# Performance work log

Measured on AMD Instinct MI355X. Metric: run time of the kernel, lower is better.

Reference implementation:

```python
import jax, jax.numpy as jnp
import numpy as np

N = 100000      # nodes
E = 1600000     # edges
IN = 128        # in_channels
H = 4           # heads
C = 16          # out_channels per head
NEG_SLOPE = 0.2 # GATConv default negative_slope


def setup_inputs() -> dict:
    key = jax.random.key(0)
    ks = jax.random.split(key, 6)
    x = jax.random.normal(ks[0], (N, IN), dtype=jnp.float32)
    edge_index = jax.random.randint(ks[1], (2, E), 0, N, dtype=jnp.int32)
    # learned params of GATConv (lin weight, att_src, att_dst, bias; concat=True)
    W = jax.random.normal(ks[2], (IN, H * C), dtype=jnp.float32) * (1.0 / np.sqrt(IN))
    att_src = jax.random.normal(ks[3], (H, C), dtype=jnp.float32) * 0.1
    att_dst = jax.random.normal(ks[4], (H, C), dtype=jnp.float32) * 0.1
    bias = jnp.zeros((H * C,), dtype=jnp.float32)
    return {"x": x, "W": W, "att_src": att_src, "att_dst": att_dst,
            "bias": bias, "edge_index": edge_index}


def reference(x, W, att_src, att_dst, bias, edge_index):
    n = x.shape[0]
    # linear transform: [N, H, C]
    xp = (x @ W).reshape(n, H, C)
    # per-node attention halves: [N, H]
    a_src = jnp.einsum('nhc,hc->nh', xp, att_src)
    a_dst = jnp.einsum('nhc,hc->nh', xp, att_dst)
    src, dst = edge_index[0], edge_index[1]
    # per-edge logits, leaky relu: [E, H]
    logits = jax.nn.leaky_relu(a_src[src] + a_dst[dst], NEG_SLOPE)
    # segment softmax over incoming edges of each dst node
    m = jax.ops.segment_max(logits, dst, num_segments=n)
    m = jnp.where(jnp.isfinite(m), m, 0.0)  # guard empty segments (-inf)
    e = jnp.exp(logits - m[dst])
    denom = jax.ops.segment_sum(e, dst, num_segments=n)
    alpha = e / (denom[dst] + 1e-16)  # [E, H]
    # message + scatter-add aggregation: [N, H, C]
    msg = xp[src] * alpha[:, :, None]
    out = jax.ops.segment_sum(msg, dst, num_segments=n).reshape(n, H * C) + bias
    return out, edge_index, alpha
```

## Files before the change

kernel.cpp:

```cpp
#include <hip/hip_runtime.h>
#include <math.h>

#define IN_CH 128
#define HCDIM 64
#define NHEAD 4
#define NEG_SLOPE 0.2f

static inline size_t align256(size_t x){ return (x + 255) & ~(size_t)255; }

__global__ __launch_bounds__(256) void gemm_att_kernel(
    const float* __restrict__ x, const float* __restrict__ W,
    const float* __restrict__ attS, const float* __restrict__ attD,
    float* __restrict__ xp, float* __restrict__ a_src, float* __restrict__ a_dst,
    int N)
{
    __shared__ __align__(16) float wlds[IN_CH * HCDIM];
    __shared__ __align__(16) float xlds[32 * 132];
    const int t = threadIdx.x;
    const int rows0 = blockIdx.x * 32;

    #pragma unroll
    for (int j = 0; j < 8; ++j) {
        int i = j * 256 + t;
        ((float4*)wlds)[i] = ((const float4*)W)[i];
    }
    #pragma unroll
    for (int j = 0; j < 4; ++j) {
        int i  = j * 256 + t;
        int r  = i >> 5;
        int kq = i & 31;
        int row = rows0 + r;
        float4 v = make_float4(0.f, 0.f, 0.f, 0.f);
        if (row < N) v = *(const float4*)&x[(size_t)row * IN_CH + kq * 4];
        *(float4*)&xlds[r * 132 + kq * 4] = v;
    }
    __syncthreads();

    const int rg = t >> 4;
    const int cg = t & 15;
    float acc0[4] = {0.f, 0.f, 0.f, 0.f};
    float acc1[4] = {0.f, 0.f, 0.f, 0.f};
    const float* xb0 = &xlds[(rg * 2 + 0) * 132];
    const float* xb1 = &xlds[(rg * 2 + 1) * 132];

    #pragma unroll 4
    for (int k = 0; k < IN_CH; ++k) {
        float4 b = *(const float4*)&wlds[k * HCDIM + cg * 4];
        float a0 = xb0[k];
        float a1 = xb1[k];
        acc0[0] = fmaf(a0, b.x, acc0[0]);
        acc0[1] = fmaf(a0, b.y, acc0[1]);
        acc0[2] = fmaf(a0, b.z, acc0[2]);
        acc0[3] = fmaf(a0, b.w, acc0[3]);
        acc1[0] = fmaf(a1, b.x, acc1[0]);
        acc1[1] = fmaf(a1, b.y, acc1[1]);
        acc1[2] = fmaf(a1, b.z, acc1[2]);
        acc1[3] = fmaf(a1, b.w, acc1[3]);
    }

    float sv[4], dv[4];
    #pragma unroll
    for (int j = 0; j < 4; ++j) { sv[j] = attS[cg * 4 + j]; dv[j] = attD[cg * 4 + j]; }

    #pragma unroll
    for (int i = 0; i < 2; ++i) {
        const float* accp = i ? acc1 : acc0;
        int row = rows0 + rg * 2 + i;
        bool ok = row < N;
        if (ok) {
            *(float4*)&xp[(size_t)row * HCDIM + cg * 4] =
                make_float4(accp[0], accp[1], accp[2], accp[3]);
        }
        float ps = accp[0]*sv[0] + accp[1]*sv[1] + accp[2]*sv[2] + accp[3]*sv[3];
        float pd = accp[0]*dv[0] + accp[1]*dv[1] + accp[2]*dv[2] + accp[3]*dv[3];
        ps += __shfl_xor(ps, 1); ps += __shfl_xor(ps, 2);
        pd += __shfl_xor(pd, 1); pd += __shfl_xor(pd, 2);
        if (ok && (cg & 3) == 0) {
            int h = cg >> 2;
            a_src[(size_t)row * NHEAD + h] = ps;
            a_dst[(size_t)row * NHEAD + h] = pd;
        }
    }
}

__global__ void hist_kernel(const int* __restrict__ dstv, int E, int* __restrict__ counts)
{
    int i = blockIdx.x * blockDim.x + threadIdx.x;
    if (i < E) atomicAdd(&counts[dstv[i]], 1);
}

__global__ __launch_bounds__(256) void scan_bsum(
    const int* __restrict__ counts, int N, int* __restrict__ bsums)
{
    __shared__ int sdata[256];
    const int b = blockIdx.x, t = threadIdx.x;
    int base = b * 2048 + t * 8;
    int s = 0;
    #pragma unroll
    for (int i = 0; i < 8; ++i) {
        int g = base + i;
        if (g < N) s += counts[g];
    }
    sdata[t] = s;
    __syncthreads();
    for (int off = 128; off > 0; off >>= 1) {
        if (t < off) sdata[t] += sdata[t + off];
        __syncthreads();
    }
    if (t == 0) bsums[b] = sdata[0];
}

__global__ void scan_offsets(const int* __restrict__ bsums, int nblk,
                             int* __restrict__ boffs, int* __restrict__ row_start,
                             int N, int E)
{
    if (threadIdx.x == 0 && blockIdx.x == 0) {
        int run = 0;
        for (int b = 0; b < nblk; ++b) { boffs[b] = run; run += bsums[b]; }
        row_start[N] = E;
    }
}

__global__ __launch_bounds__(256) void scan_write(
    const int* __restrict__ counts, int N, const int* __restrict__ boffs,
    int* __restrict__ row_start, int* __restrict__ cursor)
{
    __shared__ int tsum[256];
    __shared__ int tex[256];
    const int b = blockIdx.x, t = threadIdx.x;
    int base = b * 2048 + t * 8;
    int v[8];
    int s = 0;
    #pragma unroll
    for (int i = 0; i < 8; ++i) {
        int g = base + i;
        v[i] = (g < N) ? counts[g] : 0;
        s += v[i];
    }
    tsum[t] = s;
    __syncthreads();
    if (t == 0) {
        int run = 0;
        for (int i = 0; i < 256; ++i) { tex[i] = run; run += tsum[i]; }
    }
    __syncthreads();
    int run = boffs[b] + tex[t];
    #pragma unroll
    for (int i = 0; i < 8; ++i) {
        int g = base + i;
        if (g < N) {
            row_start[g] = run;
            cursor[g]    = run;
            run += v[i];
        }
    }
}

__global__ void scatter_kernel(const int* __restrict__ srcv, const int* __restrict__ dstv,
                               int E, int* __restrict__ cursor,
                               int* __restrict__ eid_list, int* __restrict__ src_list)
{
    int i = blockIdx.x * blockDim.x + threadIdx.x;
    if (i < E) {
        int d = dstv[i];
        int pos = atomicAdd(&cursor[d], 1);
        eid_list[pos] = i;
        src_list[pos] = srcv[i];
    }
}

__global__ void ei_to_float_kernel(const int* __restrict__ ei,
                                   float* __restrict__ out1, int n)
{
    int i = blockIdx.x * blockDim.x + threadIdx.x;
    if (i < n) out1[i] = (float)ei[i];
}

__global__ __launch_bounds__(256) void aggregate_kernel(
    const float* __restrict__ xp, const float* __restrict__ a_src,
    const float* __restrict__ a_dst, const float* __restrict__ bias,
    const int* __restrict__ row_start, const int* __restrict__ eid_list,
    const int* __restrict__ src_list,
    float* __restrict__ out, float* __restrict__ alpha_out, int N)
{
    __shared__ __align__(16) float al_f[4][256];
    __shared__ int sr[4][64];
    const int w    = threadIdx.x >> 6;
    const int lane = threadIdx.x & 63;
    const int n    = blockIdx.x * 4 + w;
    if (n >= N) return;

    const int beg = row_start[n];
    const int end = row_start[n + 1];
    const float bv = bias[lane];
    if (beg >= end) {
        out[(size_t)n * HCDIM + lane] = bv;
        return;
    }

    const float4 ad = *(const float4*)&a_dst[(size_t)n * NHEAD];

    float m0 = -INFINITY, m1 = -INFINITY, m2 = -INFINITY, m3 = -INFINITY;
    for (int cb = beg; cb < end; cb += 64) {
        int idx = cb + lane;
        if (idx < end) {
            int s = src_list[idx];
            float4 as = *(const float4*)&a_src[(size_t)s * NHEAD];
            float z0 = as.x + ad.x; z0 = z0 > 0.f ? z0 : NEG_SLOPE * z0;
            float z1 = as.y + ad.y; z1 = z1 > 0.f ? z1 : NEG_SLOPE * z1;
            float z2 = as.z + ad.z; z2 = z2 > 0.f ? z2 : NEG_SLOPE * z2;
            float z3 = as.w + ad.w; z3 = z3 > 0.f ? z3 : NEG_SLOPE * z3;
            m0 = fmaxf(m0, z0); m1 = fmaxf(m1, z1);
            m2 = fmaxf(m2, z2); m3 = fmaxf(m3, z3);
        }
    }
    #pragma unroll
    for (int off = 1; off < 64; off <<= 1) {
        m0 = fmaxf(m0, __shfl_xor(m0, off));
        m1 = fmaxf(m1, __shfl_xor(m1, off));
        m2 = fmaxf(m2, __shfl_xor(m2, off));
        m3 = fmaxf(m3, __shfl_xor(m3, off));
    }

    float t0 = 0.f, t1 = 0.f, t2 = 0.f, t3 = 0.f;
    for (int cb = beg; cb < end; cb += 64) {
        int idx = cb + lane;
        if (idx < end) {
            int s = src_list[idx];
            float4 as = *(const float4*)&a_src[(size_t)s * NHEAD];
            float z0 = as.x + ad.x; z0 = z0 > 0.f ? z0 : NEG_SLOPE * z0;
            float z1 = as.y + ad.y; z1 = z1 > 0.f ? z1 : NEG_SLOPE * z1;
            float z2 = as.z + ad.z; z2 = z2 > 0.f ? z2 : NEG_SLOPE * z2;
            float z3 = as.w + ad.w; z3 = z3 > 0.f ? z3 : NEG_SLOPE * z3;
            t0 += __expf(z0 - m0); t1 += __expf(z1 - m1);
            t2 += __expf(z2 - m2); t3 += __expf(z3 - m3);
        }
    }
    #pragma unroll
    for (int off = 1; off < 64; off <<= 1) {
        t0 += __shfl_xor(t0, off);
        t1 += __shfl_xor(t1, off);
        t2 += __shfl_xor(t2, off);
        t3 += __shfl_xor(t3, off);
    }
    const float r0 = 1.f / (t0 + 1e-16f);
    const float r1 = 1.f / (t1 + 1e-16f);
    const float r2 = 1.f / (t2 + 1e-16f);
    const float r3 = 1.f / (t3 + 1e-16f);

    const int h = lane >> 4;
    float acc = 0.f;
    for (int cb = beg; cb < end; cb += 64) {
        int idx = cb + lane;
        int nE = min(64, end - cb);
        if (idx < end) {
            int s = src_list[idx];
            float4 as = *(const float4*)&a_src[(size_t)s * NHEAD];
            float z0 = as.x + ad.x; z0 = z0 > 0.f ? z0 : NEG_SLOPE * z0;
            float z1 = as.y + ad.y; z1 = z1 > 0.f ? z1 : NEG_SLOPE * z1;
            float z2 = as.z + ad.z; z2 = z2 > 0.f ? z2 : NEG_SLOPE * z2;
            float z3 = as.w + ad.w; z3 = z3 > 0.f ? z3 : NEG_SLOPE * z3;
            float e0 = __expf(z0 - m0) * r0;
            float e1 = __expf(z1 - m1) * r1;
            float e2 = __expf(z2 - m2) * r2;
            float e3 = __expf(z3 - m3) * r3;
            int eid = eid_list[idx];
            *(float4*)&alpha_out[(size_t)eid * NHEAD] = make_float4(e0, e1, e2, e3);
            *(float4*)&al_f[w][lane * 4] = make_float4(e0, e1, e2, e3);
            sr[w][lane] = s;
        }
        for (int j = 0; j < nE; ++j) {
            float a  = al_f[w][j * 4 + h];
            int   sj = sr[w][j];
            acc = fmaf(a, xp[(size_t)sj * HCDIM + lane], acc);
        }
    }
    out[(size_t)n * HCDIM + lane] = acc + bv;
}

extern "C" void kernel_launch(void* const* d_in, const int* in_sizes, int n_in,
                              void* d_out, int out_size, void* d_ws, size_t ws_size,
                              hipStream_t stream)
{
    const float* x    = (const float*)d_in[0];
    const float* W    = (const float*)d_in[1];
    const float* attS = (const float*)d_in[2];
    const float* attD = (const float*)d_in[3];
    const float* bias = (const float*)d_in[4];
    const int*   ei   = (const int*)d_in[5];

    const int N = in_sizes[0] / IN_CH;
    const int E = in_sizes[5] / 2;
    const int* srcv = ei;
    const int* dstv = ei + E;

    char* p = (char*)d_ws;
    float* xp        = (float*)p; p += align256((size_t)N * HCDIM * 4);
    float* a_src     = (float*)p; p += align256((size_t)N * NHEAD * 4);
    float* a_dst     = (float*)p; p += align256((size_t)N * NHEAD * 4);
    int*   counts    = (int*)p;   p += align256((size_t)N * 4);
    int*   cursor    = (int*)p;   p += align256((size_t)N * 4);
    int*   row_start = (int*)p;   p += align256(((size_t)N + 1) * 4);
    int*   bsums     = (int*)p;   p += align256(1024 * 4);
    int*   boffs    = (int*)p;    p += align256(1024 * 4);
    int*   eid_list  = (int*)p;   p += align256((size_t)E * 4);
    int*   src_list  = (int*)p;   p += align256((size_t)E * 4);

    float* out       = (float*)d_out;
    float* out_ei    = out + (size_t)N * HCDIM;
    float* alpha_out = out_ei + 2 * (size_t)E;

    hipMemsetAsync(counts, 0, (size_t)N * 4, stream);

    gemm_att_kernel<<<(N + 31) / 32, 256, 0, stream>>>(
        x, W, attS, attD, xp, a_src, a_dst, N);

    hist_kernel<<<(E + 255) / 256, 256, 0, stream>>>(dstv, E, counts);

    const int nblk = (N + 2047) / 2048;
    scan_bsum<<<nblk, 256, 0, stream>>>(counts, N, bsums);
    scan_offsets<<<1, 64, 0, stream>>>(bsums, nblk, boffs, row_start, N, E);
    scan_write<<<nblk, 256, 0, stream>>>(counts, N, boffs, row_start, cursor);

    scatter_kernel<<<(E + 255) / 256, 256, 0, stream>>>(
        srcv, dstv, E, cursor, eid_list, src_list);

    aggregate_kernel<<<(N + 3) / 4, 256, 0, stream>>>(
        xp, a_src, a_dst, bias, row_start, eid_list, src_list, out, alpha_out, N);

    ei_to_float_kernel<<<(2 * E + 255) / 256, 256, 0, stream>>>(ei, out_ei, 2 * E);
}
```

Before: 427.8 us.

## Fuse front kernels, store xp in bf16, pack edge lists, add single-pass low-degree path

Merges the GEMM, degree histogram and edge-index float conversion into one launch using extra blocks. Stores the projected features in bf16 to halve gather traffic in aggregation, and packs src and edge id into one int2 list. Adds a single-pass path for nodes with degree at most 64 that computes max, sum and alpha from registers, and replaces the serial block-offset scan with a wave shuffle scan. The bf16 features reduce output precision and could break tolerance.

```diff
diff --git a/kernel.cpp b/kernel.cpp
--- a/kernel.cpp
+++ b/kernel.cpp
@@ -1,4 +1,5 @@
 #include <hip/hip_runtime.h>
+#include <hip/hip_bf16.h>
 #include <math.h>
 
 #define IN_CH 128
@@ -8,15 +9,27 @@
 
 static inline size_t align256(size_t x){ return (x + 255) & ~(size_t)255; }
 
-__global__ __launch_bounds__(256) void gemm_att_kernel(
+__device__ __forceinline__ float bf2f(__hip_bfloat16 h) { return __bfloat162float(h); }
+
+__global__ __launch_bounds__(256) void front_kernel(
     const float* __restrict__ x, const float* __restrict__ W,
     const float* __restrict__ attS, const float* __restrict__ attD,
-    float* __restrict__ xp, float* __restrict__ a_src, float* __restrict__ a_dst,
-    int N)
+    __hip_bfloat16* __restrict__ xpb, float* __restrict__ a_src, float* __restrict__ a_dst,
+    int N, int GB,
+    const int* __restrict__ ei, int E,
+    float* __restrict__ out_ei, int* __restrict__ counts)
 {
     __shared__ __align__(16) float wlds[IN_CH * HCDIM];
     __shared__ __align__(16) float xlds[32 * 132];
     const int t = threadIdx.x;
+
+    if ((int)blockIdx.x >= GB) {
+        int idx = ((int)blockIdx.x - GB) * 256 + t;
+        if (idx < 2 * E) out_ei[idx] = (float)ei[idx];
+        if (idx < E)     atomicAdd(&counts[ei[E + idx]], 1);
+        return;
+    }
+
     const int rows0 = blockIdx.x * 32;
 
     #pragma unroll
@@ -68,8 +81,14 @@
         int row = rows0 + rg * 2 + i;
         bool ok = row < N;
         if (ok) {
-            *(float4*)&xp[(size_t)row * HCDIM + cg * 4] =
-                make_float4(accp[0], accp[1], accp[2], accp[3]);
+            __hip_bfloat16 b0 = __float2bfloat16(accp[0]);
+            __hip_bfloat16 b1 = __float2bfloat16(accp[1]);
+            __hip_bfloat16 b2 = __float2bfloat16(accp[2]);
+            __hip_bfloat16 b3 = __float2bfloat16(accp[3]);
+            ushort4 pk;
+            pk.x = *(unsigned short*)&b0; pk.y = *(unsigned short*)&b1;
+            pk.z = *(unsigned short*)&b2; pk.w = *(unsigned short*)&b3;
+            *(ushort4*)&xpb[(size_t)row * HCDIM + cg * 4] = pk;
         }
         float ps = accp[0]*sv[0] + accp[1]*sv[1] + accp[2]*sv[2] + accp[3]*sv[3];
         float pd = accp[0]*dv[0] + accp[1]*dv[1] + accp[2]*dv[2] + accp[3]*dv[3];
@@ -83,12 +102,6 @@
     }
 }
 
-__global__ void hist_kernel(const int* __restrict__ dstv, int E, int* __restrict__ counts)
-{
-    int i = blockIdx.x * blockDim.x + threadIdx.x;
-    if (i < E) atomicAdd(&counts[dstv[i]], 1);
-}
-
 __global__ __launch_bounds__(256) void scan_bsum(
     const int* __restrict__ counts, int N, int* __restrict__ bsums)
 {
@@ -114,7 +127,18 @@
                              int* __restrict__ boffs, int* __restrict__ row_start,
                              int N, int E)
 {
-    if (threadIdx.x == 0 && blockIdx.x == 0) {
+    const int lane = threadIdx.x & 63;
+    if (nblk <= 64) {
+        int v = (lane < nblk) ? bsums[lane] : 0;
+        int s = v;
+        #pragma unroll
+        for (int off = 1; off < 64; off <<= 1) {
+            int u = __shfl_up(s, off);
+            if (lane >= off) s += u;
+        }
+        if (lane < nblk) boffs[lane] = s - v;
+        if (lane == 0)   row_start[N] = E;
+    } else if (lane == 0) {
         int run = 0;
         for (int b = 0; b < nblk; ++b) { boffs[b] = run; run += bsums[b]; }
         row_start[N] = E;
@@ -157,30 +181,20 @@
 }
 
 __global__ void scatter_kernel(const int* __restrict__ srcv, const int* __restrict__ dstv,
-                               int E, int* __restrict__ cursor,
-                               int* __restrict__ eid_list, int* __restrict__ src_list)
+                               int E, int* __restrict__ cursor, int2* __restrict__ plist)
 {
     int i = blockIdx.x * blockDim.x + threadIdx.x;
     if (i < E) {
         int d = dstv[i];
         int pos = atomicAdd(&cursor[d], 1);
-        eid_list[pos] = i;
-        src_list[pos] = srcv[i];
-    }
-}
-
-__global__ void ei_to_float_kernel(const int* __restrict__ ei,
-                                   float* __restrict__ out1, int n)
-{
-    int i = blockIdx.x * blockDim.x + threadIdx.x;
-    if (i < n) out1[i] = (float)ei[i];
+        plist[pos] = make_int2(srcv[i], i);
+    }
 }
 
 __global__ __launch_bounds__(256) void aggregate_kernel(
-    const float* __restrict__ xp, const float* __restrict__ a_src,
+    const __hip_bfloat16* __restrict__ xp, const float* __restrict__ a_src,
     const float* __restrict__ a_dst, const float* __restrict__ bias,
-    const int* __restrict__ row_start, const int* __restrict__ eid_list,
-    const int* __restrict__ src_list,
+    const int* __restrict__ row_start, const int2* __restrict__ plist,
     float* __restrict__ out, float* __restrict__ alpha_out, int N)
 {
     __shared__ __align__(16) float al_f[4][256];
@@ -197,15 +211,81 @@
         out[(size_t)n * HCDIM + lane] = bv;
         return;
     }
-
+    const int deg = end - beg;
     const float4 ad = *(const float4*)&a_dst[(size_t)n * NHEAD];
+    const int h = lane >> 4;
+
+    if (deg <= 64) {
+        float z0 = -INFINITY, z1 = -INFINITY, z2 = -INFINITY, z3 = -INFINITY;
+        int s = 0, eid = 0;
+        if (lane < deg) {
+            int2 pe = plist[beg + lane];
+            s = pe.x; eid = pe.y;
+            float4 as = *(const float4*)&a_src[(size_t)s * NHEAD];
+            z0 = as.x + ad.x; z0 = z0 > 0.f ? z0 : NEG_SLOPE * z0;
+            z1 = as.y + ad.y; z1 = z1 > 0.f ? z1 : NEG_SLOPE * z1;
+            z2 = as.z + ad.z; z2 = z2 > 0.f ? z2 : NEG_SLOPE * z2;
+            z3 = as.w + ad.w; z3 = z3 > 0.f ? z3 : NEG_SLOPE * z3;
+        }
+        float m0 = z0, m1 = z1, m2 = z2, m3 = z3;
+        #pragma unroll
+        for (int off = 1; off < 64; off <<= 1) {
+            m0 = fmaxf(m0, __shfl_xor(m0, off));
+            m1 = fmaxf(m1, __shfl_xor(m1, off));
+            m2 = fmaxf(m2, __shfl_xor(m2, off));
+            m3 = fmaxf(m3, __shfl_xor(m3, off));
+        }
+        float e0 = 0.f, e1 = 0.f, e2 = 0.f, e3 = 0.f;
+        if (lane < deg) {
+            e0 = __expf(z0 - m0); e1 = __expf(z1 - m1);
+            e2 = __expf(z2 - m2); e3 = __expf(z3 - m3);
+        }
+        float t0 = e0, t1 = e1, t2 = e2, t3 = e3;
+        #pragma unroll
+        for (int off = 1; off < 64; off <<= 1) {
+            t0 += __shfl_xor(t0, off);
+            t1 += __shfl_xor(t1, off);
+            t2 += __shfl_xor(t2, off);
+            t3 += __shfl_xor(t3, off);
+        }
+        if (lane < deg) {
+            e0 *= 1.f / (t0 + 1e-16f);
+            e1 *= 1.f / (t1 + 1e-16f);
+            e2 *= 1.f / (t2 + 1e-16f);
+            e3 *= 1.f / (t3 + 1e-16f);
+            *(float4*)&alpha_out[(size_t)eid * NHEAD] = make_float4(e0, e1, e2, e3);
+            *(float4*)&al_f[w][lane * 4] = make_float4(e0, e1, e2, e3);
+            sr[w][lane] = s;
+        }
+        float acc = 0.f;
+        int j = 0;
+        for (; j + 4 <= deg; j += 4) {
+            float a0 = al_f[w][(j+0) * 4 + h]; int s0 = sr[w][j+0];
+            float a1 = al_f[w][(j+1) * 4 + h]; int s1 = sr[w][j+1];
+            float a2 = al_f[w][(j+2) * 4 + h]; int s2 = sr[w][j+2];
+            float a3 = al_f[w][(j+3) * 4 + h]; int s3 = sr[w][j+3];
+            float x0 = bf2f(xp[(size_t)s0 * HCDIM + lane]);
+            float x1 = bf2f(xp[(size_t)s1 * HCDIM + lane]);
+            float x2 = bf2f(xp[(size_t)s2 * HCDIM + lane]);
+            float x3 = bf2f(xp[(size_t)s3 * HCDIM + lane]);
+            acc = fmaf(a0, x0, acc); acc = fmaf(a1, x1, acc);
+            acc = fmaf(a2, x2, acc); acc = fmaf(a3, x3, acc);
+        }
+        for (; j < deg; ++j) {
+            float a  = al_f[w][j * 4 + h];
+            int   sj = sr[w][j];
+            acc = fmaf(a, bf2f(xp[(size_t)sj * HCDIM + lane]), acc);
+        }
+        out[(size_t)n * HCDIM + lane] = acc + bv;
+        return;
+    }
 
     float m0 = -INFINITY, m1 = -INFINITY, m2 = -INFINITY, m3 = -INFINITY;
     for (int cb = beg; cb < end; cb += 64) {
         int idx = cb + lane;
         if (idx < end) {
-            int s = src_list[idx];
-            float4 as = *(const float4*)&a_src[(size_t)s * NHEAD];
+            int2 pe = plist[idx];
+            float4 as = *(const float4*)&a_src[(size_t)pe.x * NHEAD];
             float z0 = as.x + ad.x; z0 = z0 > 0.f ? z0 : NEG_SLOPE * z0;
             float z1 = as.y + ad.y; z1 = z1 > 0.f ? z1 : NEG_SLOPE * z1;
             float z2 = as.z + ad.z; z2 = z2 > 0.f ? z2 : NEG_SLOPE * z2;
@@ -221,13 +301,12 @@
         m2 = fmaxf(m2, __shfl_xor(m2, off));
         m3 = fmaxf(m3, __shfl_xor(m3, off));
     }
-
     float t0 = 0.f, t1 = 0.f, t2 = 0.f, t3 = 0.f;
     for (int cb = beg; cb < end; cb += 64) {
         int idx = cb + lane;
         if (idx < end) {
-            int s = src_list[idx];
-            float4 as = *(const float4*)&a_src[(size_t)s * NHEAD];
+            int2 pe = plist[idx];
+            float4 as = *(const float4*)&a_src[(size_t)pe.x * NHEAD];
             float z0 = as.x + ad.x; z0 = z0 > 0.f ? z0 : NEG_SLOPE * z0;
             float z1 = as.y + ad.y; z1 = z1 > 0.f ? z1 : NEG_SLOPE * z1;
             float z2 = as.z + ad.z; z2 = z2 > 0.f ? z2 : NEG_SLOPE * z2;
@@ -248,14 +327,13 @@
     const float r2 = 1.f / (t2 + 1e-16f);
     const float r3 = 1.f / (t3 + 1e-16f);
 
-    const int h = lane >> 4;
     float acc = 0.f;
     for (int cb = beg; cb < end; cb += 64) {
         int idx = cb + lane;
         int nE = min(64, end - cb);
         if (idx < end) {
-            int s = src_list[idx];
-            float4 as = *(const float4*)&a_src[(size_t)s * NHEAD];
+            int2 pe = plist[idx];
+            float4 as = *(const float4*)&a_src[(size_t)pe.x * NHEAD];
             float z0 = as.x + ad.x; z0 = z0 > 0.f ? z0 : NEG_SLOPE * z0;
             float z1 = as.y + ad.y; z1 = z1 > 0.f ? z1 : NEG_SLOPE * z1;
             float z2 = as.z + ad.z; z2 = z2 > 0.f ? z2 : NEG_SLOPE * z2;
@@ -264,15 +342,14 @@
             float e1 = __expf(z1 - m1) * r1;
             float e2 = __expf(z2 - m2) * r2;
             float e3 = __expf(z3 - m3) * r3;
-            int eid = eid_list[idx];
-            *(float4*)&alpha_out[(size_t)eid * NHEAD] = make_float4(e0, e1, e2, e3);
+            *(float4*)&alpha_out[(size_t)pe.y * NHEAD] = make_float4(e0, e1, e2, e3);
             *(float4*)&al_f[w][lane * 4] = make_float4(e0, e1, e2, e3);
-            sr[w][lane] = s;
+            sr[w][lane] = pe.x;
         }
         for (int j = 0; j < nE; ++j) {
             float a  = al_f[w][j * 4 + h];
             int   sj = sr[w][j];
-            acc = fmaf(a, xp[(size_t)sj * HCDIM + lane], acc);
+            acc = fmaf(a, bf2f(xp[(size_t)sj * HCDIM + lane]), acc);
         }
     }
     out[(size_t)n * HCDIM + lane] = acc + bv;
@@ -295,16 +372,15 @@
     const int* dstv = ei + E;
 
     char* p = (char*)d_ws;
-    float* xp        = (float*)p; p += align256((size_t)N * HCDIM * 4);
+    __hip_bfloat16* xpb = (__hip_bfloat16*)p; p += align256((size_t)N * HCDIM * 2);
     float* a_src     = (float*)p; p += align256((size_t)N * NHEAD * 4);
     float* a_dst     = (float*)p; p += align256((size_t)N * NHEAD * 4);
     int*   counts    = (int*)p;   p += align256((size_t)N * 4);
     int*   cursor    = (int*)p;   p += align256((size_t)N * 4);
     int*   row_start = (int*)p;   p += align256(((size_t)N + 1) * 4);
     int*   bsums     = (int*)p;   p += align256(1024 * 4);
-    int*   boffs    = (int*)p;    p += align256(1024 * 4);
-    int*   eid_list  = (int*)p;   p += align256((size_t)E * 4);
-    int*   src_list  = (int*)p;   p += align256((size_t)E * 4);
+    int*   boffs     = (int*)p;   p += align256(1024 * 4);
+    int2*  plist     = (int2*)p;  p += align256((size_t)E * 8);
 
     float* out       = (float*)d_out;
     float* out_ei    = out + (size_t)N * HCDIM;
@@ -312,10 +388,10 @@
 
     hipMemsetAsync(counts, 0, (size_t)N * 4, stream);
 
-    gemm_att_kernel<<<(N + 31) / 32, 256, 0, stream>>>(
-        x, W, attS, attD, xp, a_src, a_dst, N);
-
-    hist_kernel<<<(E + 255) / 256, 256, 0, stream>>>(dstv, E, counts);
+    const int GB = (N + 31) / 32;
+    const int CB = (2 * E + 255) / 256;
+    front_kernel<<<GB + CB, 256, 0, stream>>>(
+        x, W, attS, attD, xpb, a_src, a_dst, N, GB, ei, E, out_ei, counts);
 
     const int nblk = (N + 2047) / 2048;
     scan_bsum<<<nblk, 256, 0, stream>>>(counts, N, bsums);
@@ -323,10 +399,8 @@
     scan_write<<<nblk, 256, 0, stream>>>(counts, N, boffs, row_start, cursor);
 
     scatter_kernel<<<(E + 255) / 256, 256, 0, stream>>>(
-        srcv, dstv, E, cursor, eid_list, src_list);
+        srcv, dstv, E, cursor, plist);
 
     aggregate_kernel<<<(N + 3) / 4, 256, 0, stream>>>(
-        xp, a_src, a_dst, bias, row_start, eid_list, src_list, out, alpha_out, N);
-
-    ei_to_float_kernel<<<(2 * E + 255) / 256, 256, 0, stream>>>(ei, out_ei, 2 * E);
-}
+        xpb, a_src, a_dst, bias, row_start, plist, out, alpha_out, N);
+}
```

Result: faster. 414.3 us (-3.2%).
